# Performance work log

Hardware: AMD Instinct MI355X
Metric: run time of the kernel (lower is better)

## Reference

```python
import jax, jax.numpy as jnp
import numpy as np

N_NODES = 100000
NUM_ETYPE = 4
HEADS = 4
HID = 32
IN_CH = 128
EDGE_CH = 32
N_EDGES = 800000
BATCH = 1024
NEG = 5


def setup_inputs() -> dict:
    key = jax.random.key(0)
    ks = jax.random.split(key, 24)

    def w(k, shape, s=0.05):
        return jax.random.normal(k, shape, dtype=jnp.float32) * s

    inp = {}
    inp["edge_index"] = jax.random.randint(ks[0], (2, N_EDGES), 0, N_NODES)
    inp["edge_type"] = jax.random.randint(ks[1], (N_EDGES,), 0, NUM_ETYPE)
    inp["n_id"] = jax.random.randint(ks[2], (BATCH * (2 + NEG),), 0, N_NODES)
    inp["neg_sample_num"] = NEG
    inp["id_emb"] = w(ks[3], (N_NODES, IN_CH), 0.1)
    dims = [IN_CH, HEADS * HID]
    for i in range(2):
        d_in = dims[i]
        base = 4 + i * 7
        inp[f"W{i}"] = w(ks[base], (d_in, HEADS * HID))
        inp[f"Wres{i}"] = w(ks[base + 1], (d_in, HEADS * HID))
        inp[f"al{i}"] = w(ks[base + 2], (HEADS, HID))
        inp[f"ar{i}"] = w(ks[base + 3], (HEADS, HID))
        inp[f"ae{i}"] = w(ks[base + 4], (HEADS, EDGE_CH))
        inp[f"eemb{i}"] = w(ks[base + 5], (NUM_ETYPE, EDGE_CH))
        inp[f"We{i}"] = w(ks[base + 6], (EDGE_CH, HEADS * EDGE_CH))
    inp["pW1"] = w(ks[18], (2 * HEADS * HID, HID))
    inp["pb1"] = jnp.zeros((HID,), jnp.float32)
    inp["pW2"] = w(ks[19], (HID, 1))
    inp["pb2"] = jnp.zeros((1,), jnp.float32)
    return inp


def _leaky(x):
    return jnp.where(x > 0, x, 0.2 * x)  # LeakyReLU(0.2)


def _conv(h, src, dst, etype, W, Wres, al, ar, ae, eemb, We):
    """Simple-HGN style edge-typed graph attention conv with linear residual."""
    n = h.shape[0]
    feat = (h @ W).reshape(n, HEADS, HID)                      # [N,H,D]
    ef = (eemb @ We).reshape(NUM_ETYPE, HEADS, EDGE_CH)        # [T,H,De]
    el = jnp.einsum('nhd,hd->nh', feat, al)                    # [N,H]
    er = jnp.einsum('nhd,hd->nh', feat, ar)                    # [N,H]
    ee = jnp.einsum('thd,hd->th', ef, ae)                      # [T,H]
    logits = _leaky(el[src] + er[dst] + ee[etype])             # [E,H]
    # numerically stable per-destination softmax over incoming edges
    m = jax.ops.segment_max(logits, dst, num_segments=n)
    m = jnp.where(jnp.isfinite(m), m, jnp.zeros_like(m))
    a = jnp.exp(logits - m[dst])
    denom = jax.ops.segment_sum(a, dst, num_segments=n)
    alpha = a / (denom[dst] + 1e-16)                           # [E,H]
    out = jax.ops.segment_sum(feat[src] * alpha[:, :, None], dst, num_segments=n)
    return out.reshape(n, HEADS * HID) + h @ Wres


def reference(edge_index, edge_type, n_id, neg_sample_num, id_emb,
              W0, Wres0, al0, ar0, ae0, eemb0, We0,
              W1, Wres1, al1, ar1, ae1, eemb1, We1,
              pW1, pb1, pW2, pb2):
    src, dst = edge_index[0], edge_index[1]
    x = _conv(id_emb, src, dst, edge_type, W0, Wres0, al0, ar0, ae0, eemb0, We0)
    x = jax.nn.relu(x)  # relu between layers; dropout inactive at eval
    x = _conv(x, src, dst, edge_type, W1, Wres1, al1, ar1, ae1, eemb1, We1)
    b = n_id.shape[0] // (2 + neg_sample_num)
    out = x[n_id[:b]]
    pos = x[n_id[b:2 * b]]
    neg = x[n_id[2 * b:]]
    tiled = jnp.repeat(out, neg_sample_num, axis=0)  # repeat(1,neg).reshape(-1,D)

    def head(z):
        return _leaky(z @ pW1 + pb1) @ pW2 + pb2

    pos_logit = head(jnp.concatenate([out, pos], axis=-1))
    neg_logits = head(jnp.concatenate([tiled, neg], axis=-1))
    return pos_logit, neg_logits
```

## Files before the change

### kernel.cpp

```cpp
#include <hip/hip_runtime.h>
#include <hip/hip_bf16.h>
#include <math.h>

#define HEADS 4
#define HID 32
#define DIM 128
#define NEGS 5

typedef short s16x8 __attribute__((ext_vector_type(8)));
typedef short s16x4 __attribute__((ext_vector_type(4)));
typedef unsigned short u16x8 __attribute__((ext_vector_type(8)));
typedef float f32x4 __attribute__((ext_vector_type(4)));

__device__ __forceinline__ unsigned short f2bf_rn(float x) {
    unsigned int u = __float_as_uint(x);
    unsigned int r = (u + 0x7FFFu + ((u >> 16) & 1u)) >> 16;
    return (unsigned short)r;
}
__device__ __forceinline__ float bf2f(unsigned short b) {
    return __uint_as_float(((unsigned int)b) << 16);
}

__global__ void k_histflag(const int* __restrict__ src, const int* __restrict__ dst,
                           const int* __restrict__ flag2,
                           int* __restrict__ counts, int* __restrict__ flag1, int E) {
    int e = blockIdx.x * 256 + threadIdx.x;
    if (e < E) {
        int d = dst[e];
        atomicAdd(&counts[d], 1);
        if (flag2[d]) flag1[src[e]] = 1;
    }
}

__global__ __launch_bounds__(1024) void k_scanA(const int* __restrict__ counts,
                                                int* __restrict__ rowtmp,
                                                int* __restrict__ bsum, int N) {
    __shared__ int s[1024];
    int i = blockIdx.x * 1024 + threadIdx.x;
    int v = (i < N) ? counts[i] : 0;
    s[threadIdx.x] = v;
    __syncthreads();
    for (int off = 1; off < 1024; off <<= 1) {
        int t = (threadIdx.x >= off) ? s[threadIdx.x - off] : 0;
        __syncthreads();
        s[threadIdx.x] += t;
        __syncthreads();
    }
    if (i < N) rowtmp[i] = s[threadIdx.x];
    if (threadIdx.x == 1023) bsum[blockIdx.x] = s[1023];
}

__global__ void k_scanB(const int* __restrict__ bsum, int* __restrict__ bsumex, int nb) {
    int l = threadIdx.x;
    int a = (2 * l < nb) ? bsum[2 * l] : 0;
    int b = (2 * l + 1 < nb) ? bsum[2 * l + 1] : 0;
    int s = a + b;
    for (int off = 1; off < 64; off <<= 1) {
        int t = __shfl_up(s, off);
        if (l >= off) s += t;
    }
    int excl = s - (a + b);
    if (2 * l < nb) bsumex[2 * l] = excl;
    if (2 * l + 1 < nb) bsumex[2 * l + 1] = excl + a;
}

__global__ void k_scanC(const int* __restrict__ rowtmp, const int* __restrict__ counts,
                        const int* __restrict__ bsumex, int* __restrict__ row_start,
                        int* __restrict__ cursor, int N) {
    int i = blockIdx.x * 256 + threadIdx.x;
    if (i < N) {
        int st = rowtmp[i] - counts[i] + bsumex[i >> 10];
        row_start[i] = st;
        cursor[i] = st;
    }
}

__global__ void k_scatter(const int* __restrict__ dst, int* __restrict__ cursor,
                          int* __restrict__ csr_edge, int E) {
    int e = blockIdx.x * 256 + threadIdx.x;
    if (e < E) {
        int p = atomicAdd(&cursor[dst[e]], 1);
        csr_edge[p] = e;
    }
}

__global__ void k_flag2(const int* __restrict__ n_id, int* __restrict__ flag2,
                        int* __restrict__ flag1, int M) {
    int i = blockIdx.x * 256 + threadIdx.x;
    if (i < M) { int n = n_id[i]; flag2[n] = 1; flag1[n] = 1; }
}

__global__ void k_compact(const int* __restrict__ flag1, const int* __restrict__ flag2,
                          int* __restrict__ list1, int* __restrict__ list2,
                          int* __restrict__ cnt1, int* __restrict__ cnt2, int N) {
    int i = blockIdx.x * 256 + threadIdx.x;
    int lane = threadIdx.x & 63;
    unsigned long long lt = (lane == 63) ? ~0ull >> 1 : (1ull << lane) - 1;

    bool a = (i < N) && flag1[i];
    unsigned long long m = __ballot(a);
    int base = 0;
    if (lane == 0 && m) base = atomicAdd(cnt1, __popcll(m));
    base = __shfl(base, 0);
    if (a) list1[base + __popcll(m & lt)] = i;

    bool b = (i < N) && flag2[i];
    m = __ballot(b);
    base = 0;
    if (lane == 0 && m) base = atomicAdd(cnt2, __popcll(m));
    base = __shfl(base, 0);
    if (b) list2[base + __popcll(m & lt)] = i;
}

__global__ void k_wcvt(const float* __restrict__ W0, const float* __restrict__ Wres0,
                       const float* __restrict__ W1, const float* __restrict__ Wres1,
                       unsigned short* __restrict__ bt) {
    int idx = blockIdx.x * 256 + threadIdx.x;
    int layer = idx >> 15;
    int r = idx & 32767;
    int k = r >> 8;
    int n = r & 255;
    const float* src = layer ? ((n < 128) ? W1 : Wres1) : ((n < 128) ? W0 : Wres0);
    float x = src[k * 128 + (n & 127)];
    unsigned short h = f2bf_rn(x);
    unsigned short l = f2bf_rn(x - bf2f(h));
    unsigned short* base = bt + (size_t)layer * 2 * 32768;
    base[n * 128 + k] = h;
    base[32768 + n * 128 + k] = l;
}

__global__ __launch_bounds__(256, 4) void k_gemm_fused(const float* __restrict__ A,
                                                       const unsigned short* __restrict__ Bhi,
                                                       const unsigned short* __restrict__ Blo,
                                                       unsigned short* __restrict__ featb,
                                                       float* __restrict__ res,
                                                       const float* __restrict__ al,
                                                       const float* __restrict__ ar,
                                                       float* __restrict__ el,
                                                       float* __restrict__ er,
                                                       const int* __restrict__ rowlist,
                                                       const int* __restrict__ rowcnt,
                                                       const int* __restrict__ resflag,
                                                       int N) {
    int limit = rowcnt ? *rowcnt : N;
    int c = blockIdx.x;
    int m0 = blockIdx.y * 64;
    if (m0 >= limit) return;

    __shared__ unsigned short Bh[8192];
    __shared__ unsigned short Bl[8192];
    int tid = threadIdx.x;
    int lane = tid & 63, w = tid >> 6;
    int wm = (w & 1) * 32, wn = (w >> 1) * 32;
    int lr = lane & 15, g = lane >> 4;

#pragma unroll
    for (int i = 0; i < 4; ++i) {
        int f = tid + i * 256;
        int row = f >> 4, g16 = f & 15;
        int off = (row * 256 + ((g16 * 16) ^ ((row & 7) << 4))) >> 1;
        *(u16x8*)&Bh[off] = *(const u16x8*)(Bhi + (size_t)(c * 64 + row) * DIM + g16 * 8);
        *(u16x8*)&Bl[off] = *(const u16x8*)(Blo + (size_t)(c * 64 + row) * DIM + g16 * 8);
    }

    s16x8 afh[2][4], afl[2][4];
#pragma unroll
    for (int fm = 0; fm < 2; ++fm) {
        int idx = m0 + wm + fm * 16 + lr;
        bool valid = idx < limit;
        int grow = 0;
        if (valid) grow = rowlist ? rowlist[idx] : idx;
        const float* ap = A + (size_t)grow * DIM;
#pragma unroll
        for (int ks = 0; ks < 4; ++ks) {
            float4 p = make_float4(0.f, 0.f, 0.f, 0.f);
            float4 q = make_float4(0.f, 0.f, 0.f, 0.f);
            if (valid) {
                p = *(const float4*)(ap + ks * 32 + g * 4);
                q = *(const float4*)(ap + ks * 32 + 16 + g * 4);
            }
            float vv[8] = {p.x, p.y, p.z, p.w, q.x, q.y, q.z, q.w};
            s16x8 hv, lv;
#pragma unroll
            for (int j = 0; j < 8; ++j) {
                unsigned short h = f2bf_rn(vv[j]);
                hv[j] = (short)h;
                lv[j] = (short)f2bf_rn(vv[j] - bf2f(h));
            }
            afh[fm][ks] = hv;
            afl[fm][ks] = lv;
        }
    }
    __syncthreads();

    f32x4 acc[2][2];
#pragma unroll
    for (int fm = 0; fm < 2; ++fm)
#pragma unroll
        for (int fn = 0; fn < 2; ++fn) acc[fm][fn] = (f32x4){0.f, 0.f, 0.f, 0.f};

#pragma unroll
    for (int ks = 0; ks < 4; ++ks) {
        s16x8 bfh[2], bfl[2];
#pragma unroll
        for (int fn = 0; fn < 2; ++fn) {
            int row = wn + fn * 16 + lr;
            int sw = (row & 7) << 4;
            int o1 = (row * 256 + ((ks * 64 + g * 8) ^ sw)) >> 1;
            int o2 = (row * 256 + ((ks * 64 + 32 + g * 8) ^ sw)) >> 1;
            s16x4 p = *(const s16x4*)&Bh[o1];
            s16x4 q = *(const s16x4*)&Bh[o2];
            bfh[fn] = (s16x8){p[0], p[1], p[2], p[3], q[0], q[1], q[2], q[3]};
            p = *(const s16x4*)&Bl[o1];
            q = *(const s16x4*)&Bl[o2];
            bfl[fn] = (s16x8){p[0], p[1], p[2], p[3], q[0], q[1], q[2], q[3]};
        }
#pragma unroll
        for (int fm = 0; fm < 2; ++fm)
#pragma unroll
            for (int fn = 0; fn < 2; ++fn) {
                acc[fm][fn] = __builtin_amdgcn_mfma_f32_16x16x32_bf16(afh[fm][ks], bfh[fn], acc[fm][fn], 0, 0, 0);
                acc[fm][fn] = __builtin_amdgcn_mfma_f32_16x16x32_bf16(afh[fm][ks], bfl[fn], acc[fm][fn], 0, 0, 0);
                acc[fm][fn] = __builtin_amdgcn_mfma_f32_16x16x32_bf16(afl[fm][ks], bfh[fn], acc[fm][fn], 0, 0, 0);
            }
    }

#pragma unroll
    for (int fm = 0; fm < 2; ++fm)
#pragma unroll
        for (int fn = 0; fn < 2; ++fn) {
            int idx0 = m0 + wm + fm * 16 + g * 4;
            int dc = ((c * 64) & 127) + wn + fn * 16 + lr;
#pragma unroll
            for (int r = 0; r < 4; ++r) {
                int idx = idx0 + r;
                if (idx < limit) {
                    int gr = rowlist ? rowlist[idx] : idx;
                    if (c < 2) {
                        featb[(size_t)gr * DIM + dc] = f2bf_rn(acc[fm][fn][r]);
                    } else if (!resflag || resflag[gr]) {
                        res[(size_t)gr * DIM + dc] = acc[fm][fn][r];
                    }
                }
            }
        }

    if (c < 2) {
        int h = c * 2 + (wn >> 5);
        float a0 = al[h * HID + lr], a1 = al[h * HID + 16 + lr];
        float b0 = ar[h * HID + lr], b1 = ar[h * HID + 16 + lr];
#pragma unroll
        for (int fm = 0; fm < 2; ++fm)
#pragma unroll
            for (int r = 0; r < 4; ++r) {
                float ev = acc[fm][0][r] * a0 + acc[fm][1][r] * a1;
                float rv = acc[fm][0][r] * b0 + acc[fm][1][r] * b1;
#pragma unroll
                for (int off = 1; off < 16; off <<= 1) {
                    ev += __shfl_xor(ev, off);
                    rv += __shfl_xor(rv, off);
                }
                if (lr == 0) {
                    int idx = m0 + wm + fm * 16 + g * 4 + r;
                    if (idx < limit) {
                        int node = rowlist ? rowlist[idx] : idx;
                        el[node * 4 + h] = ev;
                        er[node * 4 + h] = rv;
                    }
                }
            }
    }
}

__global__ void k_ee(const float* __restrict__ eemb, const float* __restrict__ We,
                     const float* __restrict__ ae, float* __restrict__ ee) {
    int t = threadIdx.x;
    if (t >= 16) return;
    int et = t >> 2, h = t & 3;
    float s = 0.f;
    for (int d = 0; d < 32; ++d) {
        float ef = 0.f;
        for (int k = 0; k < 32; ++k) ef += eemb[et * 32 + k] * We[k * DIM + h * 32 + d];
        s += ef * ae[h * 32 + d];
    }
    ee[t] = s;
}

template <int RELU>
__global__ __launch_bounds__(256) void k_agg(const unsigned short* __restrict__ featb,
                                             const float* __restrict__ el,
                                             const float* __restrict__ er,
                                             const float* __restrict__ eeB,
                                             const int* __restrict__ srcArr,
                                             const int* __restrict__ etArr,
                                             const int* __restrict__ csr_edge,
                                             const int* __restrict__ row_start,
                                             const int* __restrict__ counts,
                                             const int* __restrict__ dlist,
                                             const int* __restrict__ dcnt,
                                             float* __restrict__ out) {
    int wv = threadIdx.x >> 6;
    int lane = threadIdx.x & 63;
    int idx = blockIdx.x * 4 + wv;
    if (idx >= *dcnt) return;
    int node = dlist[idx];

    int beg = row_start[node];
    int deg = counts[node];
    int eh = lane & 3;
    float er_v = er[node * 4 + eh];

    float m = -INFINITY;
    for (int base = 0; base < deg; base += 16) {
        int ei = base + (lane >> 2);
        float lg = -INFINITY;
        if (ei < deg) {
            int e = csr_edge[beg + ei];
            float x = el[srcArr[e] * 4 + eh] + er_v + eeB[etArr[e] * 4 + eh];
            lg = (x > 0.f) ? x : 0.2f * x;
        }
        m = fmaxf(m, lg);
    }
    for (int off = 4; off < 64; off <<= 1) m = fmaxf(m, __shfl_xor(m, off));

    float denom = 0.f, acc0 = 0.f, acc1 = 0.f;
    int h1 = lane >> 5;
    for (int base = 0; base < deg; base += 16) {
        int ei = base + (lane >> 2);
        float wgt = 0.f;
        int s = 0;
        if (ei < deg) {
            int e = csr_edge[beg + ei];
            s = srcArr[e];
            float x = el[s * 4 + eh] + er_v + eeB[etArr[e] * 4 + eh];
            x = (x > 0.f) ? x : 0.2f * x;
            wgt = expf(x - m);
            denom += wgt;
        }
        int cnt = min(16, deg - base);
        for (int j = 0; j < cnt; ++j) {
            int sj = __shfl(s, j * 4);
            float w1 = __shfl(wgt, j * 4 + h1);
            float w2 = __shfl(wgt, j * 4 + 2 + h1);
            acc0 += w1 * bf2f(featb[(size_t)sj * DIM + lane]);
            acc1 += w2 * bf2f(featb[(size_t)sj * DIM + 64 + lane]);
        }
    }
    for (int off = 4; off < 64; off <<= 1) denom += __shfl_xor(denom, off);
    float d1 = __shfl(denom, h1);
    float d2 = __shfl(denom, 2 + h1);

    float r0 = out[(size_t)node * DIM + lane] + acc0 / (d1 + 1e-16f);
    float r1 = out[(size_t)node * DIM + 64 + lane] + acc1 / (d2 + 1e-16f);
    if (RELU) { r0 = fmaxf(r0, 0.f); r1 = fmaxf(r1, 0.f); }
    out[(size_t)node * DIM + lane] = r0;
    out[(size_t)node * DIM + 64 + lane] = r1;
}

__global__ __launch_bounds__(256) void k_head(const float* __restrict__ x1,
                                              const int* __restrict__ n_id,
                                              const float* __restrict__ pW1,
                                              const float* __restrict__ pb1,
                                              const float* __restrict__ pW2,
                                              const float* __restrict__ pb2,
                                              float* __restrict__ dout, int B) {
    int o = blockIdx.x * 4 + (threadIdx.x >> 6);
    int lane = threadIdx.x & 63;
    int total = B + B * NEGS;
    if (o >= total) return;
    int a, c;
    if (o < B) { a = n_id[o]; c = n_id[B + o]; }
    else { int j = o - B; a = n_id[j / NEGS]; c = n_id[2 * B + j]; }

    int j = lane & 31;
    int half = lane >> 5;
    int row = half ? c : a;
    const float* z = x1 + (size_t)row * DIM;
    const float* w = pW1 + (half ? 128 * 32 : 0);
    float t = 0.f;
#pragma unroll 8
    for (int k = 0; k < 128; ++k) t += z[k] * w[k * 32 + j];
    t += __shfl_xor(t, 32);
    t += pb1[j];
    t = (t > 0.f) ? t : 0.2f * t;
    float r = t * pW2[j];
    for (int off = 1; off < 32; off <<= 1) r += __shfl_xor(r, off);
    if (lane == 0) dout[o] = r + pb2[0];
}

extern "C" void kernel_launch(void* const* d_in, const int* in_sizes, int n_in,
                              void* d_out, int out_size, void* d_ws, size_t ws_size,
                              hipStream_t stream) {
    const int* edge_index = (const int*)d_in[0];
    const int* etype      = (const int*)d_in[1];
    const int* n_id       = (const int*)d_in[2];
    const float* id_emb   = (const float*)d_in[4];
    const float* W0    = (const float*)d_in[5];
    const float* Wres0 = (const float*)d_in[6];
    const float* al0   = (const float*)d_in[7];
    const float* ar0   = (const float*)d_in[8];
    const float* ae0   = (const float*)d_in[9];
    const float* eemb0 = (const float*)d_in[10];
    const float* We0   = (const float*)d_in[11];
    const float* W1    = (const float*)d_in[12];
    const float* Wres1 = (const float*)d_in[13];
    const float* al1   = (const float*)d_in[14];
    const float* ar1   = (const float*)d_in[15];
    const float* ae1   = (const float*)d_in[16];
    const float* eemb1 = (const float*)d_in[17];
    const float* We1   = (const float*)d_in[18];
    const float* pW1   = (const float*)d_in[19];
    const float* pb1   = (const float*)d_in[20];
    const float* pW2   = (const float*)d_in[21];
    const float* pb2   = (const float*)d_in[22];

    int E = in_sizes[1];
    int N = in_sizes[4] / DIM;
    int M = in_sizes[2];
    int B = M / (2 + NEGS);
    const int* srcArr = edge_index;
    const int* dstArr = edge_index + E;

    size_t N128 = (size_t)N * DIM;
    unsigned short* featb = (unsigned short*)d_ws;
    float* x0   = (float*)(featb + N128);
    float* x1   = x0 + N128;
    float* el   = x1 + N128;
    float* er   = el + (size_t)N * 4;
    float* eeB  = er + (size_t)N * 4;
    int* counts    = (int*)(eeB + 32);
    int* flag1     = counts + N;
    int* flag2     = flag1 + N;
    int* cnt1      = flag2 + N;
    int* cnt2      = cnt1 + 1;
    int* rowtmp    = cnt2 + 1;
    int* row_start = rowtmp + N;
    int* cursor    = row_start + N;
    int* csr_edge  = cursor + N;
    int* list1     = csr_edge + E;
    int* list2     = list1 + N;
    int* bsum      = list2 + M;
    int* bsumex    = bsum + 256;
    unsigned short* bt = (unsigned short*)(bsumex + 256);

    k_wcvt<<<256, 256, 0, stream>>>(W0, Wres0, W1, Wres1, bt);
    hipMemsetAsync(counts, 0, (size_t)(3 * N + 2) * sizeof(int), stream);

    k_flag2<<<(M + 255) / 256, 256, 0, stream>>>(n_id, flag2, flag1, M);
    k_histflag<<<(E + 255) / 256, 256, 0, stream>>>(srcArr, dstArr, flag2, counts, flag1, E);

    int nb = (N + 1023) / 1024;
    k_scanA<<<nb, 1024, 0, stream>>>(counts, rowtmp, bsum, N);
    k_scanB<<<1, 64, 0, stream>>>(bsum, bsumex, nb);
    k_scanC<<<(N + 255) / 256, 256, 0, stream>>>(rowtmp, counts, bsumex, row_start, cursor, N);
    k_scatter<<<(E + 255) / 256, 256, 0, stream>>>(dstArr, cursor, csr_edge, E);
    k_compact<<<(N + 255) / 256, 256, 0, stream>>>(flag1, flag2, list1, list2, cnt1, cnt2, N);

    dim3 ggrid(4, (N + 63) / 64);
    int aggGridFull = (N + 3) / 4;
    int aggGridS2 = (M + 3) / 4;

    k_gemm_fused<<<ggrid, 256, 0, stream>>>(id_emb, bt, bt + 32768, featb, x0,
                                            al0, ar0, el, er, nullptr, nullptr, flag1, N);
    k_ee<<<1, 16, 0, stream>>>(eemb0, We0, ae0, eeB);
    k_agg<1><<<aggGridFull, 256, 0, stream>>>(featb, el, er, eeB, srcArr, etype, csr_edge,
                                              row_start, counts, list1, cnt1, x0);

    k_gemm_fused<<<ggrid, 256, 0, stream>>>(x0, bt + 65536, bt + 98304, featb, x1,
                                            al1, ar1, el, er, list1, cnt1, flag2, N);
    k_ee<<<1, 16, 0, stream>>>(eemb1, We1, ae1, eeB);
    k_agg<0><<<aggGridS2, 256, 0, stream>>>(featb, el, er, eeB, srcArr, etype, csr_edge,
                                            row_start, counts, list2, cnt2, x1);

    int total = B * (1 + NEGS);
    k_head<<<(total + 3) / 4, 256, 0, stream>>>(x1, n_id, pW1, pb1, pW2, pb2,
                                                (float*)d_out, B);
}
```

Baseline: 387.1 us.

## Persistent GEMM with full weight matrix in LDS and atomic strip scheduling

Replaces the 4-column-block GEMM grid with a persistent 256-block kernel of 1024 threads. Each block loads the full 256-column hi/lo bf16 weight matrix into 128KB of LDS once. Waves then grab 16-row strips through an atomic counter, so each A row is read and split-converted once instead of four times. The weights are stored permuted so each B fragment is a single 16-byte LDS load. This cuts redundant A traffic and B tile reloads, at the cost of one block per CU, more registers per wave, and contention on the atomic counter.

```diff
diff --git a/kernel.cpp b/kernel.cpp
--- a/kernel.cpp
+++ b/kernel.cpp
@@ -8,7 +8,6 @@
 #define NEGS 5
 
 typedef short s16x8 __attribute__((ext_vector_type(8)));
-typedef short s16x4 __attribute__((ext_vector_type(4)));
 typedef unsigned short u16x8 __attribute__((ext_vector_type(8)));
 typedef float f32x4 __attribute__((ext_vector_type(4)));
 
@@ -124,58 +123,74 @@
     float x = src[k * 128 + (n & 127)];
     unsigned short h = f2bf_rn(x);
     unsigned short l = f2bf_rn(x - bf2f(h));
+    int ks = k >> 5, kr = k & 31;
+    int slot = (kr < 16) ? (ks * 32 + (kr >> 2) * 8 + (kr & 3))
+                         : (ks * 32 + ((kr - 16) >> 2) * 8 + 4 + ((kr - 16) & 3));
     unsigned short* base = bt + (size_t)layer * 2 * 32768;
-    base[n * 128 + k] = h;
-    base[32768 + n * 128 + k] = l;
-}
-
-__global__ __launch_bounds__(256, 4) void k_gemm_fused(const float* __restrict__ A,
-                                                       const unsigned short* __restrict__ Bhi,
-                                                       const unsigned short* __restrict__ Blo,
-                                                       unsigned short* __restrict__ featb,
-                                                       float* __restrict__ res,
-                                                       const float* __restrict__ al,
-                                                       const float* __restrict__ ar,
-                                                       float* __restrict__ el,
-                                                       float* __restrict__ er,
-                                                       const int* __restrict__ rowlist,
-                                                       const int* __restrict__ rowcnt,
-                                                       const int* __restrict__ resflag,
-                                                       int N) {
-    int limit = rowcnt ? *rowcnt : N;
-    int c = blockIdx.x;
-    int m0 = blockIdx.y * 64;
-    if (m0 >= limit) return;
-
-    __shared__ unsigned short Bh[8192];
-    __shared__ unsigned short Bl[8192];
+    base[n * 128 + slot] = h;
+    base[32768 + n * 128 + slot] = l;
+}
+
+template <int HASLIST>
+__global__ __launch_bounds__(1024)
+void k_gemm_cu(const float* __restrict__ A,
+               const unsigned short* __restrict__ Bhi,
+               const unsigned short* __restrict__ Blo,
+               unsigned short* __restrict__ featb,
+               float* __restrict__ res,
+               const float* __restrict__ al,
+               const float* __restrict__ ar,
+               float* __restrict__ el,
+               float* __restrict__ er,
+               const int* __restrict__ rowlist,
+               const int* __restrict__ rowcnt,
+               const int* __restrict__ resflag,
+               int* __restrict__ wctr,
+               int N) {
+    int limit = HASLIST ? *rowcnt : N;
+    __shared__ unsigned short Bh[32768];
+    __shared__ unsigned short Bl[32768];
     int tid = threadIdx.x;
-    int lane = tid & 63, w = tid >> 6;
-    int wm = (w & 1) * 32, wn = (w >> 1) * 32;
-    int lr = lane & 15, g = lane >> 4;
 
 #pragma unroll
     for (int i = 0; i < 4; ++i) {
-        int f = tid + i * 256;
+        int f = tid + i * 1024;
         int row = f >> 4, g16 = f & 15;
         int off = (row * 256 + ((g16 * 16) ^ ((row & 7) << 4))) >> 1;
-        *(u16x8*)&Bh[off] = *(const u16x8*)(Bhi + (size_t)(c * 64 + row) * DIM + g16 * 8);
-        *(u16x8*)&Bl[off] = *(const u16x8*)(Blo + (size_t)(c * 64 + row) * DIM + g16 * 8);
-    }
-
-    s16x8 afh[2][4], afl[2][4];
-#pragma unroll
-    for (int fm = 0; fm < 2; ++fm) {
-        int idx = m0 + wm + fm * 16 + lr;
-        bool valid = idx < limit;
-        int grow = 0;
-        if (valid) grow = rowlist ? rowlist[idx] : idx;
-        const float* ap = A + (size_t)grow * DIM;
+        *(u16x8*)&Bh[off] = *(const u16x8*)(Bhi + row * 128 + g16 * 8);
+        *(u16x8*)&Bl[off] = *(const u16x8*)(Blo + row * 128 + g16 * 8);
+    }
+    __syncthreads();
+
+    int lane = tid & 63;
+    int lr = lane & 15, g = lane >> 4;
+
+    float ew0[4], ew1[4], rw0[4], rw1[4];
+#pragma unroll
+    for (int h = 0; h < 4; ++h) {
+        ew0[h] = al[h * HID + lr]; ew1[h] = al[h * HID + 16 + lr];
+        rw0[h] = ar[h * HID + lr]; rw1[h] = ar[h * HID + 16 + lr];
+    }
+
+    int nStrips = (limit + 15) >> 4;
+    for (;;) {
+        int s;
+        if (lane == 0) s = atomicAdd(wctr, 1);
+        s = __shfl(s, 0);
+        if (s >= nStrips) break;
+        int m0 = s * 16;
+
+        int aidx = m0 + lr;
+        bool avalid = aidx < limit;
+        int agrow = 0;
+        if (avalid) agrow = HASLIST ? rowlist[aidx] : aidx;
+        const float* ap = A + (size_t)agrow * DIM;
+        s16x8 afh[4], afl[4];
 #pragma unroll
         for (int ks = 0; ks < 4; ++ks) {
             float4 p = make_float4(0.f, 0.f, 0.f, 0.f);
             float4 q = make_float4(0.f, 0.f, 0.f, 0.f);
-            if (valid) {
+            if (avalid) {
                 p = *(const float4*)(ap + ks * 32 + g * 4);
                 q = *(const float4*)(ap + ks * 32 + 16 + g * 4);
             }
@@ -183,92 +198,77 @@
             s16x8 hv, lv;
 #pragma unroll
             for (int j = 0; j < 8; ++j) {
-                unsigned short h = f2bf_rn(vv[j]);
-                hv[j] = (short)h;
-                lv[j] = (short)f2bf_rn(vv[j] - bf2f(h));
+                unsigned short hh = f2bf_rn(vv[j]);
+                hv[j] = (short)hh;
+                lv[j] = (short)f2bf_rn(vv[j] - bf2f(hh));
             }
-            afh[fm][ks] = hv;
-            afl[fm][ks] = lv;
-        }
-    }
-    __syncthreads();
-
-    f32x4 acc[2][2];
-#pragma unroll
-    for (int fm = 0; fm < 2; ++fm)
-#pragma unroll
-        for (int fn = 0; fn < 2; ++fn) acc[fm][fn] = (f32x4){0.f, 0.f, 0.f, 0.f};
-
-#pragma unroll
-    for (int ks = 0; ks < 4; ++ks) {
-        s16x8 bfh[2], bfl[2];
-#pragma unroll
-        for (int fn = 0; fn < 2; ++fn) {
-            int row = wn + fn * 16 + lr;
-            int sw = (row & 7) << 4;
-            int o1 = (row * 256 + ((ks * 64 + g * 8) ^ sw)) >> 1;
-            int o2 = (row * 256 + ((ks * 64 + 32 + g * 8) ^ sw)) >> 1;
-            s16x4 p = *(const s16x4*)&Bh[o1];
-            s16x4 q = *(const s16x4*)&Bh[o2];
-            bfh[fn] = (s16x8){p[0], p[1], p[2], p[3], q[0], q[1], q[2], q[3]};
-            p = *(const s16x4*)&Bl[o1];
-            q = *(const s16x4*)&Bl[o2];
-            bfl[fn] = (s16x8){p[0], p[1], p[2], p[3], q[0], q[1], q[2], q[3]};
-        }
-#pragma unroll
-        for (int fm = 0; fm < 2; ++fm)
-#pragma unroll
-            for (int fn = 0; fn < 2; ++fn) {
-                acc[fm][fn] = __builtin_amdgcn_mfma_f32_16x16x32_bf16(afh[fm][ks], bfh[fn], acc[fm][fn], 0, 0, 0);
-                acc[fm][fn] = __builtin_amdgcn_mfma_f32_16x16x32_bf16(afh[fm][ks], bfl[fn], acc[fm][fn], 0, 0, 0);
-                acc[fm][fn] = __builtin_amdgcn_mfma_f32_16x16x32_bf16(afl[fm][ks], bfh[fn], acc[fm][fn], 0, 0, 0);
-            }
-    }
-
-#pragma unroll
-    for (int fm = 0; fm < 2; ++fm)
-#pragma unroll
-        for (int fn = 0; fn < 2; ++fn) {
-            int idx0 = m0 + wm + fm * 16 + g * 4;
-            int dc = ((c * 64) & 127) + wn + fn * 16 + lr;
-#pragma unroll
-            for (int r = 0; r < 4; ++r) {
-                int idx = idx0 + r;
-                if (idx < limit) {
-                    int gr = rowlist ? rowlist[idx] : idx;
-                    if (c < 2) {
-                        featb[(size_t)gr * DIM + dc] = f2bf_rn(acc[fm][fn][r]);
-                    } else if (!resflag || resflag[gr]) {
-                        res[(size_t)gr * DIM + dc] = acc[fm][fn][r];
-                    }
+            afh[ks] = hv;
+            afl[ks] = lv;
+        }
+
+        int orow[4];
+        bool ovalid[4];
+#pragma unroll
+        for (int r = 0; r < 4; ++r) {
+            int idx2 = m0 + g * 4 + r;
+            ovalid[r] = idx2 < limit;
+            orow[r] = 0;
+            if (ovalid[r]) orow[r] = HASLIST ? rowlist[idx2] : idx2;
+        }
+
+#pragma unroll
+        for (int ch = 0; ch < 2; ++ch) {
+            f32x4 acc[8];
+#pragma unroll
+            for (int cf = 0; cf < 8; ++cf) acc[cf] = (f32x4){0.f, 0.f, 0.f, 0.f};
+
+#pragma unroll
+            for (int ks = 0; ks < 4; ++ks) {
+#pragma unroll
+                for (int cf = 0; cf < 8; ++cf) {
+                    int brow = ch * 128 + cf * 16 + lr;
+                    int off = (brow * 256 + ((ks * 64 + g * 16) ^ ((brow & 7) << 4))) >> 1;
+                    s16x8 bh = *(const s16x8*)&Bh[off];
+                    s16x8 bl = *(const s16x8*)&Bl[off];
+                    acc[cf] = __builtin_amdgcn_mfma_f32_16x16x32_bf16(afh[ks], bh, acc[cf], 0, 0, 0);
+                    acc[cf] = __builtin_amdgcn_mfma_f32_16x16x32_bf16(afh[ks], bl, acc[cf], 0, 0, 0);
+                    acc[cf] = __builtin_amdgcn_mfma_f32_16x16x32_bf16(afl[ks], bh, acc[cf], 0, 0, 0);
                 }
             }
-        }
-
-    if (c < 2) {
-        int h = c * 2 + (wn >> 5);
-        float a0 = al[h * HID + lr], a1 = al[h * HID + 16 + lr];
-        float b0 = ar[h * HID + lr], b1 = ar[h * HID + 16 + lr];
-#pragma unroll
-        for (int fm = 0; fm < 2; ++fm)
-#pragma unroll
-            for (int r = 0; r < 4; ++r) {
-                float ev = acc[fm][0][r] * a0 + acc[fm][1][r] * a1;
-                float rv = acc[fm][0][r] * b0 + acc[fm][1][r] * b1;
-#pragma unroll
-                for (int off = 1; off < 16; off <<= 1) {
-                    ev += __shfl_xor(ev, off);
-                    rv += __shfl_xor(rv, off);
-                }
-                if (lr == 0) {
-                    int idx = m0 + wm + fm * 16 + g * 4 + r;
-                    if (idx < limit) {
-                        int node = rowlist ? rowlist[idx] : idx;
-                        el[node * 4 + h] = ev;
-                        er[node * 4 + h] = rv;
+
+            if (ch == 0) {
+#pragma unroll
+                for (int cf = 0; cf < 8; ++cf)
+#pragma unroll
+                    for (int r = 0; r < 4; ++r)
+                        if (ovalid[r])
+                            featb[(size_t)orow[r] * DIM + cf * 16 + lr] = f2bf_rn(acc[cf][r]);
+#pragma unroll
+                for (int h = 0; h < 4; ++h)
+#pragma unroll
+                    for (int r = 0; r < 4; ++r) {
+                        float ev = acc[2 * h][r] * ew0[h] + acc[2 * h + 1][r] * ew1[h];
+                        float rv = acc[2 * h][r] * rw0[h] + acc[2 * h + 1][r] * rw1[h];
+#pragma unroll
+                        for (int off = 1; off < 16; off <<= 1) {
+                            ev += __shfl_xor(ev, off);
+                            rv += __shfl_xor(rv, off);
+                        }
+                        if (lr == 0 && ovalid[r]) {
+                            el[orow[r] * 4 + h] = ev;
+                            er[orow[r] * 4 + h] = rv;
+                        }
                     }
-                }
+            } else {
+#pragma unroll
+                for (int r = 0; r < 4; ++r)
+                    if (ovalid[r] && (!resflag || resflag[orow[r]])) {
+#pragma unroll
+                        for (int cf = 0; cf < 8; ++cf)
+                            res[(size_t)orow[r] * DIM + cf * 16 + lr] = acc[cf][r];
+                    }
             }
+        }
     }
 }
 
@@ -433,7 +433,9 @@
     int* flag2     = flag1 + N;
     int* cnt1      = flag2 + N;
     int* cnt2      = cnt1 + 1;
-    int* rowtmp    = cnt2 + 1;
+    int* wctr0     = cnt2 + 1;
+    int* wctr1     = wctr0 + 1;
+    int* rowtmp    = wctr1 + 1;
     int* row_start = rowtmp + N;
     int* cursor    = row_start + N;
     int* csr_edge  = cursor + N;
@@ -444,7 +446,7 @@
     unsigned short* bt = (unsigned short*)(bsumex + 256);
 
     k_wcvt<<<256, 256, 0, stream>>>(W0, Wres0, W1, Wres1, bt);
-    hipMemsetAsync(counts, 0, (size_t)(3 * N + 2) * sizeof(int), stream);
+    hipMemsetAsync(counts, 0, (size_t)(3 * N + 4) * sizeof(int), stream);
 
     k_flag2<<<(M + 255) / 256, 256, 0, stream>>>(n_id, flag2, flag1, M);
     k_histflag<<<(E + 255) / 256, 256, 0, stream>>>(srcArr, dstArr, flag2, counts, flag1, E);
@@ -456,18 +458,19 @@
     k_scatter<<<(E + 255) / 256, 256, 0, stream>>>(dstArr, cursor, csr_edge, E);
     k_compact<<<(N + 255) / 256, 256, 0, stream>>>(flag1, flag2, list1, list2, cnt1, cnt2, N);
 
-    dim3 ggrid(4, (N + 63) / 64);
     int aggGridFull = (N + 3) / 4;
     int aggGridS2 = (M + 3) / 4;
 
-    k_gemm_fused<<<ggrid, 256, 0, stream>>>(id_emb, bt, bt + 32768, featb, x0,
-                                            al0, ar0, el, er, nullptr, nullptr, flag1, N);
+    k_gemm_cu<0><<<256, 1024, 0, stream>>>(id_emb, bt, bt + 32768,
+                                           featb, x0, al0, ar0, el, er,
+                                           nullptr, nullptr, flag1, wctr0, N);
     k_ee<<<1, 16, 0, stream>>>(eemb0, We0, ae0, eeB);
     k_agg<1><<<aggGridFull, 256, 0, stream>>>(featb, el, er, eeB, srcArr, etype, csr_edge,
                                               row_start, counts, list1, cnt1, x0);
 
-    k_gemm_fused<<<ggrid, 256, 0, stream>>>(x0, bt + 65536, bt + 98304, featb, x1,
-                                            al1, ar1, el, er, list1, cnt1, flag2, N);
+    k_gemm_cu<1><<<256, 1024, 0, stream>>>(x0, bt + 65536, bt + 98304,
+                                           featb, x1, al1, ar1, el, er,
+                                           list1, cnt1, flag2, wctr1, N);
     k_ee<<<1, 16, 0, stream>>>(eemb1, We1, ae1, eeB);
     k_agg<0><<<aggGridS2, 256, 0, stream>>>(featb, el, er, eeB, srcArr, etype, csr_edge,
                                             row_start, counts, list2, cnt2, x1);
```

After: 469.7 us. 21.3% more time.

## Merge setup kernels, fold scan/compact, drop LDS B staging in GEMM

Applied to the files above, without the earlier changes.

Weight conversion, buffer zeroing and both edge-type attention terms now run in one setup kernel, replacing a memset and two tiny kernels. The block-sum scan and node-list compaction are folded into the scan finalize kernel. The GEMM no longer stages B in shared memory. It pre-permutes the B layout so each lane loads its MFMA fragment with one 16-byte global load, and it raises the occupancy hint. Together these cut launch count and LDS sync, at the cost of redundant global/L2 reads of B across waves and a redundant block-sum scan in every scanC block.

```diff
diff --git a/kernel.cpp b/kernel.cpp
--- a/kernel.cpp
+++ b/kernel.cpp
@@ -8,7 +8,6 @@
 #define NEGS 5
 
 typedef short s16x8 __attribute__((ext_vector_type(8)));
-typedef short s16x4 __attribute__((ext_vector_type(4)));
 typedef unsigned short u16x8 __attribute__((ext_vector_type(8)));
 typedef float f32x4 __attribute__((ext_vector_type(4)));
 
@@ -19,6 +18,57 @@
 }
 __device__ __forceinline__ float bf2f(unsigned short b) {
     return __uint_as_float(((unsigned int)b) << 16);
+}
+
+__global__ void k_setup(const float* __restrict__ W0, const float* __restrict__ Wres0,
+                        const float* __restrict__ W1, const float* __restrict__ Wres1,
+                        const float* __restrict__ eemb0, const float* __restrict__ We0,
+                        const float* __restrict__ ae0,
+                        const float* __restrict__ eemb1, const float* __restrict__ We1,
+                        const float* __restrict__ ae1,
+                        unsigned short* __restrict__ bt, float* __restrict__ eeB,
+                        int* __restrict__ zbase, int zn) {
+    int idx = blockIdx.x * 256 + threadIdx.x;
+
+    for (int i = idx; i < zn; i += 65536) zbase[i] = 0;
+
+    {
+        int layer = idx >> 15;
+        int r = idx & 32767;
+        int k = r >> 8;
+        int n = r & 255;
+        const float* src = layer ? ((n < 128) ? W1 : Wres1) : ((n < 128) ? W0 : Wres0);
+        float x = src[k * 128 + (n & 127)];
+        unsigned short h = f2bf_rn(x);
+        unsigned short l = f2bf_rn(x - bf2f(h));
+        int ks = k >> 5, kr = k & 31;
+        int slot = (kr < 16) ? (ks * 32 + (kr >> 2) * 8 + (kr & 3))
+                             : (ks * 32 + ((kr - 16) >> 2) * 8 + 4 + ((kr - 16) & 3));
+        unsigned short* base = bt + (size_t)layer * 2 * 32768;
+        base[n * 128 + slot] = h;
+        base[32768 + n * 128 + slot] = l;
+    }
+
+    if (idx < 32) {
+        int layer = idx >> 4, t = idx & 15;
+        const float* eemb = layer ? eemb1 : eemb0;
+        const float* We   = layer ? We1 : We0;
+        const float* ae   = layer ? ae1 : ae0;
+        int et = t >> 2, h = t & 3;
+        float s = 0.f;
+        for (int d = 0; d < 32; ++d) {
+            float ef = 0.f;
+            for (int k = 0; k < 32; ++k) ef += eemb[et * 32 + k] * We[k * DIM + h * 32 + d];
+            s += ef * ae[h * 32 + d];
+        }
+        eeB[layer * 16 + t] = s;
+    }
+}
+
+__global__ void k_flag2(const int* __restrict__ n_id, int* __restrict__ flag2,
+                        int* __restrict__ flag1, int M) {
+    int i = blockIdx.x * 256 + threadIdx.x;
+    if (i < M) { int n = n_id[i]; flag2[n] = 1; flag1[n] = 1; }
 }
 
 __global__ void k_histflag(const int* __restrict__ src, const int* __restrict__ dst,
@@ -50,29 +100,56 @@
     if (threadIdx.x == 1023) bsum[blockIdx.x] = s[1023];
 }
 
-__global__ void k_scanB(const int* __restrict__ bsum, int* __restrict__ bsumex, int nb) {
-    int l = threadIdx.x;
-    int a = (2 * l < nb) ? bsum[2 * l] : 0;
-    int b = (2 * l + 1 < nb) ? bsum[2 * l + 1] : 0;
-    int s = a + b;
-    for (int off = 1; off < 64; off <<= 1) {
-        int t = __shfl_up(s, off);
-        if (l >= off) s += t;
-    }
-    int excl = s - (a + b);
-    if (2 * l < nb) bsumex[2 * l] = excl;
-    if (2 * l + 1 < nb) bsumex[2 * l + 1] = excl + a;
-}
-
-__global__ void k_scanC(const int* __restrict__ rowtmp, const int* __restrict__ counts,
-                        const int* __restrict__ bsumex, int* __restrict__ row_start,
-                        int* __restrict__ cursor, int N) {
-    int i = blockIdx.x * 256 + threadIdx.x;
+__global__ __launch_bounds__(256) void k_scanC(const int* __restrict__ rowtmp,
+                                               const int* __restrict__ counts,
+                                               const int* __restrict__ bsum, int nb,
+                                               int* __restrict__ row_start,
+                                               int* __restrict__ cursor,
+                                               const int* __restrict__ flag1,
+                                               const int* __restrict__ flag2,
+                                               int* __restrict__ list1,
+                                               int* __restrict__ list2,
+                                               int* __restrict__ cnt1,
+                                               int* __restrict__ cnt2, int N) {
+    __shared__ int sex[128];
+    int tid = threadIdx.x;
+    if (tid < 64) {
+        int l = tid;
+        int a = (2 * l < nb) ? bsum[2 * l] : 0;
+        int b = (2 * l + 1 < nb) ? bsum[2 * l + 1] : 0;
+        int s = a + b;
+        for (int off = 1; off < 64; off <<= 1) {
+            int t = __shfl_up(s, off);
+            if (l >= off) s += t;
+        }
+        int excl = s - (a + b);
+        sex[2 * l] = excl;
+        sex[2 * l + 1] = excl + a;
+    }
+    __syncthreads();
+
+    int i = blockIdx.x * 256 + tid;
+    int lane = tid & 63;
     if (i < N) {
-        int st = rowtmp[i] - counts[i] + bsumex[i >> 10];
+        int st = rowtmp[i] - counts[i] + sex[i >> 10];
         row_start[i] = st;
         cursor[i] = st;
     }
+
+    unsigned long long lt = (lane == 63) ? ~0ull >> 1 : (1ull << lane) - 1;
+    bool a = (i < N) && flag1[i];
+    unsigned long long m = __ballot(a);
+    int base = 0;
+    if (lane == 0 && m) base = atomicAdd(cnt1, __popcll(m));
+    base = __shfl(base, 0);
+    if (a) list1[base + __popcll(m & lt)] = i;
+
+    bool b = (i < N) && flag2[i];
+    m = __ballot(b);
+    base = 0;
+    if (lane == 0 && m) base = atomicAdd(cnt2, __popcll(m));
+    base = __shfl(base, 0);
+    if (b) list2[base + __popcll(m & lt)] = i;
 }
 
 __global__ void k_scatter(const int* __restrict__ dst, int* __restrict__ cursor,
@@ -84,92 +161,38 @@
     }
 }
 
-__global__ void k_flag2(const int* __restrict__ n_id, int* __restrict__ flag2,
-                        int* __restrict__ flag1, int M) {
-    int i = blockIdx.x * 256 + threadIdx.x;
-    if (i < M) { int n = n_id[i]; flag2[n] = 1; flag1[n] = 1; }
-}
-
-__global__ void k_compact(const int* __restrict__ flag1, const int* __restrict__ flag2,
-                          int* __restrict__ list1, int* __restrict__ list2,
-                          int* __restrict__ cnt1, int* __restrict__ cnt2, int N) {
-    int i = blockIdx.x * 256 + threadIdx.x;
-    int lane = threadIdx.x & 63;
-    unsigned long long lt = (lane == 63) ? ~0ull >> 1 : (1ull << lane) - 1;
-
-    bool a = (i < N) && flag1[i];
-    unsigned long long m = __ballot(a);
-    int base = 0;
-    if (lane == 0 && m) base = atomicAdd(cnt1, __popcll(m));
-    base = __shfl(base, 0);
-    if (a) list1[base + __popcll(m & lt)] = i;
-
-    bool b = (i < N) && flag2[i];
-    m = __ballot(b);
-    base = 0;
-    if (lane == 0 && m) base = atomicAdd(cnt2, __popcll(m));
-    base = __shfl(base, 0);
-    if (b) list2[base + __popcll(m & lt)] = i;
-}
-
-__global__ void k_wcvt(const float* __restrict__ W0, const float* __restrict__ Wres0,
-                       const float* __restrict__ W1, const float* __restrict__ Wres1,
-                       unsigned short* __restrict__ bt) {
-    int idx = blockIdx.x * 256 + threadIdx.x;
-    int layer = idx >> 15;
-    int r = idx & 32767;
-    int k = r >> 8;
-    int n = r & 255;
-    const float* src = layer ? ((n < 128) ? W1 : Wres1) : ((n < 128) ? W0 : Wres0);
-    float x = src[k * 128 + (n & 127)];
-    unsigned short h = f2bf_rn(x);
-    unsigned short l = f2bf_rn(x - bf2f(h));
-    unsigned short* base = bt + (size_t)layer * 2 * 32768;
-    base[n * 128 + k] = h;
-    base[32768 + n * 128 + k] = l;
-}
-
-__global__ __launch_bounds__(256, 4) void k_gemm_fused(const float* __restrict__ A,
-                                                       const unsigned short* __restrict__ Bhi,
-                                                       const unsigned short* __restrict__ Blo,
-                                                       unsigned short* __restrict__ featb,
-                                                       float* __restrict__ res,
-                                                       const float* __restrict__ al,
-                                                       const float* __restrict__ ar,
-                                                       float* __restrict__ el,
-                                                       float* __restrict__ er,
-                                                       const int* __restrict__ rowlist,
-                                                       const int* __restrict__ rowcnt,
-                                                       const int* __restrict__ resflag,
-                                                       int N) {
-    int limit = rowcnt ? *rowcnt : N;
+template <int HASLIST>
+__global__ __launch_bounds__(256, 6)
+void k_gemm_ng(const float* __restrict__ A,
+               const unsigned short* __restrict__ Bhi,
+               const unsigned short* __restrict__ Blo,
+               unsigned short* __restrict__ featb,
+               float* __restrict__ res,
+               const float* __restrict__ al,
+               const float* __restrict__ ar,
+               float* __restrict__ el,
+               float* __restrict__ er,
+               const int* __restrict__ rowlist,
+               const int* __restrict__ rowcnt,
+               const int* __restrict__ resflag,
+               int N) {
+    int limit = HASLIST ? *rowcnt : N;
     int c = blockIdx.x;
     int m0 = blockIdx.y * 64;
     if (m0 >= limit) return;
 
-    __shared__ unsigned short Bh[8192];
-    __shared__ unsigned short Bl[8192];
     int tid = threadIdx.x;
     int lane = tid & 63, w = tid >> 6;
     int wm = (w & 1) * 32, wn = (w >> 1) * 32;
     int lr = lane & 15, g = lane >> 4;
 
-#pragma unroll
-    for (int i = 0; i < 4; ++i) {
-        int f = tid + i * 256;
-        int row = f >> 4, g16 = f & 15;
-        int off = (row * 256 + ((g16 * 16) ^ ((row & 7) << 4))) >> 1;
-        *(u16x8*)&Bh[off] = *(const u16x8*)(Bhi + (size_t)(c * 64 + row) * DIM + g16 * 8);
-        *(u16x8*)&Bl[off] = *(const u16x8*)(Blo + (size_t)(c * 64 + row) * DIM + g16 * 8);
-    }
-
     s16x8 afh[2][4], afl[2][4];
 #pragma unroll
     for (int fm = 0; fm < 2; ++fm) {
         int idx = m0 + wm + fm * 16 + lr;
         bool valid = idx < limit;
         int grow = 0;
-        if (valid) grow = rowlist ? rowlist[idx] : idx;
+        if (valid) grow = HASLIST ? rowlist[idx] : idx;
         const float* ap = A + (size_t)grow * DIM;
 #pragma unroll
         for (int ks = 0; ks < 4; ++ks) {
@@ -183,15 +206,14 @@
             s16x8 hv, lv;
 #pragma unroll
             for (int j = 0; j < 8; ++j) {
-                unsigned short h = f2bf_rn(vv[j]);
-                hv[j] = (short)h;
-                lv[j] = (short)f2bf_rn(vv[j] - bf2f(h));
+                unsigned short hh = f2bf_rn(vv[j]);
+                hv[j] = (short)hh;
+                lv[j] = (short)f2bf_rn(vv[j] - bf2f(hh));
             }
             afh[fm][ks] = hv;
             afl[fm][ks] = lv;
         }
     }
-    __syncthreads();
 
     f32x4 acc[2][2];
 #pragma unroll
@@ -204,16 +226,10 @@
         s16x8 bfh[2], bfl[2];
 #pragma unroll
         for (int fn = 0; fn < 2; ++fn) {
-            int row = wn + fn * 16 + lr;
-            int sw = (row & 7) << 4;
-            int o1 = (row * 256 + ((ks * 64 + g * 8) ^ sw)) >> 1;
-            int o2 = (row * 256 + ((ks * 64 + 32 + g * 8) ^ sw)) >> 1;
-            s16x4 p = *(const s16x4*)&Bh[o1];
-            s16x4 q = *(const s16x4*)&Bh[o2];
-            bfh[fn] = (s16x8){p[0], p[1], p[2], p[3], q[0], q[1], q[2], q[3]};
-            p = *(const s16x4*)&Bl[o1];
-            q = *(const s16x4*)&Bl[o2];
-            bfl[fn] = (s16x8){p[0], p[1], p[2], p[3], q[0], q[1], q[2], q[3]};
+            int brow = c * 64 + wn + fn * 16 + lr;
+            size_t o = (size_t)brow * DIM + ks * 32 + g * 8;
+            bfh[fn] = (s16x8)(*(const u16x8*)(Bhi + o));
+            bfl[fn] = (s16x8)(*(const u16x8*)(Blo + o));
         }
 #pragma unroll
         for (int fm = 0; fm < 2; ++fm)
@@ -235,7 +251,7 @@
             for (int r = 0; r < 4; ++r) {
                 int idx = idx0 + r;
                 if (idx < limit) {
-                    int gr = rowlist ? rowlist[idx] : idx;
+                    int gr = HASLIST ? rowlist[idx] : idx;
                     if (c < 2) {
                         featb[(size_t)gr * DIM + dc] = f2bf_rn(acc[fm][fn][r]);
                     } else if (!resflag || resflag[gr]) {
@@ -263,27 +279,13 @@
                 if (lr == 0) {
                     int idx = m0 + wm + fm * 16 + g * 4 + r;
                     if (idx < limit) {
-                        int node = rowlist ? rowlist[idx] : idx;
+                        int node = HASLIST ? rowlist[idx] : idx;
                         el[node * 4 + h] = ev;
                         er[node * 4 + h] = rv;
                     }
                 }
             }
     }
-}
-
-__global__ void k_ee(const float* __restrict__ eemb, const float* __restrict__ We,
-                     const float* __restrict__ ae, float* __restrict__ ee) {
-    int t = threadIdx.x;
-    if (t >= 16) return;
-    int et = t >> 2, h = t & 3;
-    float s = 0.f;
-    for (int d = 0; d < 32; ++d) {
-        float ef = 0.f;
-        for (int k = 0; k < 32; ++k) ef += eemb[et * 32 + k] * We[k * DIM + h * 32 + d];
-        s += ef * ae[h * 32 + d];
-    }
-    ee[t] = s;
 }
 
 template <int RELU>
@@ -440,36 +442,34 @@
     int* list1     = csr_edge + E;
     int* list2     = list1 + N;
     int* bsum      = list2 + M;
-    int* bsumex    = bsum + 256;
-    unsigned short* bt = (unsigned short*)(bsumex + 256);
-
-    k_wcvt<<<256, 256, 0, stream>>>(W0, Wres0, W1, Wres1, bt);
-    hipMemsetAsync(counts, 0, (size_t)(3 * N + 2) * sizeof(int), stream);
+    unsigned short* bt = (unsigned short*)(bsum + 256);
+
+    k_setup<<<256, 256, 0, stream>>>(W0, Wres0, W1, Wres1,
+                                     eemb0, We0, ae0, eemb1, We1, ae1,
+                                     bt, eeB, counts, 3 * N + 2);
 
     k_flag2<<<(M + 255) / 256, 256, 0, stream>>>(n_id, flag2, flag1, M);
     k_histflag<<<(E + 255) / 256, 256, 0, stream>>>(srcArr, dstArr, flag2, counts, flag1, E);
-
     int nb = (N + 1023) / 1024;
     k_scanA<<<nb, 1024, 0, stream>>>(counts, rowtmp, bsum, N);
-    k_scanB<<<1, 64, 0, stream>>>(bsum, bsumex, nb);
-    k_scanC<<<(N + 255) / 256, 256, 0, stream>>>(rowtmp, counts, bsumex, row_start, cursor, N);
+    k_scanC<<<(N + 255) / 256, 256, 0, stream>>>(rowtmp, counts, bsum, nb, row_start, cursor,
+                                                 flag1, flag2, list1, list2, cnt1, cnt2, N);
     k_scatter<<<(E + 255) / 256, 256, 0, stream>>>(dstArr, cursor, csr_edge, E);
-    k_compact<<<(N + 255) / 256, 256, 0, stream>>>(flag1, flag2, list1, list2, cnt1, cnt2, N);
 
     dim3 ggrid(4, (N + 63) / 64);
     int aggGridFull = (N + 3) / 4;
     int aggGridS2 = (M + 3) / 4;
 
-    k_gemm_fused<<<ggrid, 256, 0, stream>>>(id_emb, bt, bt + 32768, featb, x0,
-                                            al0, ar0, el, er, nullptr, nullptr, flag1, N);
-    k_ee<<<1, 16, 0, stream>>>(eemb0, We0, ae0, eeB);
+    k_gemm_ng<0><<<ggrid, 256, 0, stream>>>(id_emb, bt, bt + 32768,
+                                            featb, x0, al0, ar0, el, er,
+                                            nullptr, nullptr, flag1, N);
     k_agg<1><<<aggGridFull, 256, 0, stream>>>(featb, el, er, eeB, srcArr, etype, csr_edge,
                                               row_start, counts, list1, cnt1, x0);
 
-    k_gemm_fused<<<ggrid, 256, 0, stream>>>(x0, bt + 65536, bt + 98304, featb, x1,
-                                            al1, ar1, el, er, list1, cnt1, flag2, N);
-    k_ee<<<1, 16, 0, stream>>>(eemb1, We1, ae1, eeB);
-    k_agg<0><<<aggGridS2, 256, 0, stream>>>(featb, el, er, eeB, srcArr, etype, csr_edge,
+    k_gemm_ng<1><<<ggrid, 256, 0, stream>>>(x0, bt + 65536, bt + 98304,
+                                            featb, x1, al1, ar1, el, er,
+                                            list1, cnt1, flag2, N);
+    k_agg<0><<<aggGridS2, 256, 0, stream>>>(featb, el, er, eeB + 16, srcArr, etype, csr_edge,
                                             row_start, counts, list2, cnt2, x1);
 
     int total = B * (1 + NEGS);
```

Result: slower. 484.6 us (+25.2%).
